# Kernel optimization log

Hardware: AMD Instinct MI355X
Metric: run time of the kernel (lower is better)

Reference implementation:

```python
import jax, jax.numpy as jnp
import numpy as np

B = 32768      # batch
D = 512        # embedding dim
V = 100000     # vocab_length (row 0 reserved -> table has V+1 rows)
S = 100        # num_neg_samples (hard-coded in source)
DISTORTION = 0.4


def _expected_counts():
    # fixed_unigram sampler: zipf-ish counts, distorted by 0.4, 1 reserved id
    counts = 1.0 / np.arange(1, V + 1, dtype=np.float64)
    p = counts ** DISTORTION
    p = p / p.sum()
    q = np.zeros(V + 1, dtype=np.float64)
    # unique sampling expected count: E[id in sample] = 1-(1-p)^S
    q[1:] = -np.expm1(S * np.log1p(-p))
    q[0] = 1e-9  # reserved id, never sampled; avoid log(0)
    return q


def setup_inputs() -> dict:
    key = jax.random.key(0)
    k1, k2, k3, k4 = jax.random.split(key, 4)
    label = jax.random.randint(k1, (B,), 1, V + 1, dtype=jnp.int64)
    inputs = jax.random.normal(k2, (B, D), dtype=jnp.float32)
    weights = jax.random.normal(k3, (V + 1, D), dtype=jnp.float32) * 0.05
    biases = jnp.zeros((V + 1,), dtype=jnp.float32)
    sampled_ids = jax.random.choice(k4, V, (S,), replace=False).astype(jnp.int64) + 1
    q = jnp.asarray(_expected_counts(), dtype=jnp.float32)
    true_expected_count = q[label]          # [B]
    sampled_expected_count = q[sampled_ids]  # [S]
    return {
        "label": label, "inputs": inputs, "weights": weights, "biases": biases,
        "sampled_ids": sampled_ids,
        "true_expected_count": true_expected_count,
        "sampled_expected_count": sampled_expected_count,
    }


def reference(label, inputs, weights, biases, sampled_ids,
              true_expected_count, sampled_expected_count):
    # --- _compute_sampled_logits with subtract_log_q=True ---
    true_w = weights[label]                                   # [B, D] gather
    true_logits = (jnp.einsum('bd,bd->b', inputs, true_w)
                   + biases[label]
                   - jnp.log(true_expected_count))            # [B]
    samp_w = weights[sampled_ids]                             # [S, D] gather
    samp_logits = (jnp.einsum('bd,sd->bs', inputs, samp_w)
                   + biases[sampled_ids]
                   - jnp.log(sampled_expected_count))         # [B, S]
    logits = jnp.concatenate([true_logits[:, None], samp_logits], axis=1)  # [B, 1+S]
    # labels are one-hot at column 0 -> CE = logsumexp - true logit
    losses = jax.nn.logsumexp(logits, axis=1) - logits[:, 0]
    loss = jnp.mean(losses)
    return logits, loss
```

## Files before the change

### kernel.cpp

```cpp
#include <hip/hip_runtime.h>
#include <math.h>

#define B_TOT 32768
#define DIM   512
#define NS    100
#define NCOL  101
#define TB    128
#define NBLK  (B_TOT / TB)
#define WPITCH 520

typedef __attribute__((ext_vector_type(8))) short short8;
typedef __attribute__((ext_vector_type(4))) float f32x4;

static __device__ __forceinline__ short f2bf(float f) {
    unsigned u = __builtin_bit_cast(unsigned, f);
    unsigned r = (u + 0x7FFFu + ((u >> 16) & 1u)) >> 16;
    return (short)r;
}

__global__ __launch_bounds__(512)
void fused_kernel(const int* __restrict__ label,
                  const float* __restrict__ inputs,
                  const float* __restrict__ weights,
                  const float* __restrict__ biases,
                  const int* __restrict__ sampled_ids,
                  const float* __restrict__ tq,
                  const float* __restrict__ sq,
                  float* __restrict__ out,
                  float* __restrict__ partial)
{
    __shared__ short W_lds[112 * WPITCH];
    __shared__ float base_lds[112];
    __shared__ float tl_lds[TB];
    __shared__ float ls_lds[8];

    const int t = threadIdx.x;

    for (int idx = t; idx < NS * (DIM / 4); idx += 512) {
        const int row = idx >> 7;
        const int kq  = (idx & 127) * 4;
        const float4 wv = *(const float4*)(weights + (long)sampled_ids[row] * DIM + kq);
        short4 p = make_short4(f2bf(wv.x), f2bf(wv.y), f2bf(wv.z), f2bf(wv.w));
        *(short4*)&W_lds[row * WPITCH + kq] = p;
    }
    if (t < 112)
        base_lds[t] = (t < NS) ? biases[sampled_ids[t]] - logf(sq[t]) : -INFINITY;

    const int wave = t >> 6;
    const int lane = t & 63;
    const int rit  = lane & 15;
    const int seg  = lane >> 4;
    const int absRow = blockIdx.x * TB + wave * 16 + rit;
    const int lab = label[absRow];
    const float* aptr = inputs  + (long)absRow * DIM + seg * 8;
    const float* wtp  = weights + (long)lab    * DIM + seg * 8;

    __syncthreads();

    f32x4 acc[7];
    #pragma unroll
    for (int c = 0; c < 7; c++) acc[c] = (f32x4){0.f, 0.f, 0.f, 0.f};
    float tacc = 0.f;

    #pragma unroll
    for (int kc = 0; kc < DIM / 32; kc++) {
        const int k0 = kc * 32;
        const float4 a0 = *(const float4*)(aptr + k0);
        const float4 a1 = *(const float4*)(aptr + k0 + 4);
        const float4 w0 = *(const float4*)(wtp + k0);
        const float4 w1 = *(const float4*)(wtp + k0 + 4);

        tacc = fmaf(a0.x, w0.x, tacc); tacc = fmaf(a0.y, w0.y, tacc);
        tacc = fmaf(a0.z, w0.z, tacc); tacc = fmaf(a0.w, w0.w, tacc);
        tacc = fmaf(a1.x, w1.x, tacc); tacc = fmaf(a1.y, w1.y, tacc);
        tacc = fmaf(a1.z, w1.z, tacc); tacc = fmaf(a1.w, w1.w, tacc);

        short8 af;
        af[0] = f2bf(a0.x); af[1] = f2bf(a0.y); af[2] = f2bf(a0.z); af[3] = f2bf(a0.w);
        af[4] = f2bf(a1.x); af[5] = f2bf(a1.y); af[6] = f2bf(a1.z); af[7] = f2bf(a1.w);

        const int wko = k0 + seg * 8;
        #pragma unroll
        for (int c = 0; c < 7; c++) {
            const short8 bf = *(const short8*)&W_lds[(c * 16 + rit) * WPITCH + wko];
            acc[c] = __builtin_amdgcn_mfma_f32_16x16x32_bf16(af, bf, acc[c], 0, 0, 0);
        }
    }

    tacc += __shfl_xor(tacc, 16);
    tacc += __shfl_xor(tacc, 32);
    const float tl = tacc + biases[lab] - logf(tq[absRow]);
    if (lane < 16) {
        tl_lds[wave * 16 + lane] = tl;
        out[(long)absRow * NCOL] = tl;
    }
    __syncthreads();

    const int g = lane >> 4;
    float loss_sum = 0.f;
    #pragma unroll
    for (int i = 0; i < 4; i++) {
        const int r = g * 4 + i;
        const long orow = (long)(blockIdx.x * TB + wave * 16 + r) * NCOL;
        const float tlv = tl_lds[wave * 16 + r];
        float v[7];
        float m = tlv;
        #pragma unroll
        for (int c = 0; c < 7; c++) {
            const int col = c * 16 + rit;
            v[c] = (col < NS) ? acc[c][i] + base_lds[col] : -INFINITY;
            m = fmaxf(m, v[c]);
        }
        #pragma unroll
        for (int off = 1; off < 16; off <<= 1) m = fmaxf(m, __shfl_xor(m, off));
        float s = (rit == 0) ? expf(tlv - m) : 0.f;
        #pragma unroll
        for (int c = 0; c < 7; c++) s += expf(v[c] - m);
        #pragma unroll
        for (int off = 1; off < 16; off <<= 1) s += __shfl_xor(s, off);
        loss_sum += m + logf(s) - tlv;
        #pragma unroll
        for (int c = 0; c < 7; c++) {
            const int col = c * 16 + rit;
            if (col < NS) out[orow + 1 + col] = v[c];
        }
    }
    float wl = (rit == 0) ? loss_sum : 0.f;
    wl += __shfl_xor(wl, 16);
    wl += __shfl_xor(wl, 32);
    if (lane == 0) ls_lds[wave] = wl;
    __syncthreads();
    if (t == 0) {
        float bp = 0.f;
        #pragma unroll
        for (int w = 0; w < 8; w++) bp += ls_lds[w];
        partial[blockIdx.x] = bp;
    }
}

__global__ __launch_bounds__(256)
void reduce_kernel(const float* __restrict__ partial, float* __restrict__ out_loss)
{
    __shared__ double buf[256];
    buf[threadIdx.x] = (double)partial[threadIdx.x];
    __syncthreads();
    for (int o = 128; o > 0; o >>= 1) {
        if (threadIdx.x < o) buf[threadIdx.x] += buf[threadIdx.x + o];
        __syncthreads();
    }
    if (threadIdx.x == 0) *out_loss = (float)(buf[0] * (1.0 / (double)B_TOT));
}

extern "C" void kernel_launch(void* const* d_in, const int* in_sizes, int n_in,
                              void* d_out, int out_size, void* d_ws, size_t ws_size,
                              hipStream_t stream)
{
    const int*   label   = (const int*)d_in[0];
    const float* inputs  = (const float*)d_in[1];
    const float* weights = (const float*)d_in[2];
    const float* biases  = (const float*)d_in[3];
    const int*   sids    = (const int*)d_in[4];
    const float* tq      = (const float*)d_in[5];
    const float* sq      = (const float*)d_in[6];
    float* out     = (float*)d_out;
    float* partial = (float*)d_ws;

    fused_kernel<<<NBLK, 512, 0, stream>>>(label, inputs, weights, biases,
                                           sids, tq, sq, out, partial);
    reduce_kernel<<<1, 256, 0, stream>>>(partial, out + (long)B_TOT * NCOL);
}
```

Measured before the change: 40.74 us.

## Prepack sampled weights into MFMA fragment layout in a separate kernel

A new pack kernel gathers the sampled weight rows once, converts them to bf16 and stores them in global memory already arranged in the per-lane MFMA B-fragment order. The bias-minus-log-q terms are precomputed there too. The fused kernel then reads these fragments straight from global memory (L2-resident) instead of having every block gather and convert 100 rows into LDS. This removes the LDS footprint and the block barriers, which should raise occupancy (launch bounds now ask for 4 blocks). In exchange it adds a third kernel launch and per-iteration global loads in the MFMA loop.

```diff
diff --git a/kernel.cpp b/kernel.cpp
--- a/kernel.cpp
+++ b/kernel.cpp
@@ -7,7 +7,10 @@
 #define NCOL  101
 #define TB    128
 #define NBLK  (B_TOT / TB)
-#define WPITCH 520
+
+#define BASE_OFF 28672
+#define LPART_OFF 28800
+#define NPACK (16 * 7 * 64)
 
 typedef __attribute__((ext_vector_type(8))) short short8;
 typedef __attribute__((ext_vector_type(4))) float f32x4;
@@ -18,34 +21,42 @@
     return (short)r;
 }
 
-__global__ __launch_bounds__(512)
+__global__ __launch_bounds__(256)
+void pack_kernel(const float* __restrict__ weights, const float* __restrict__ biases,
+                 const int* __restrict__ sids, const float* __restrict__ sq,
+                 short* __restrict__ wpack, float* __restrict__ base_g)
+{
+    const int tid = blockIdx.x * 256 + threadIdx.x;
+    if (tid < 112)
+        base_g[tid] = (tid < NS) ? biases[sids[tid]] - logf(sq[tid]) : -INFINITY;
+    if (tid >= NPACK) return;
+    const int kc = tid / 448, rem = tid % 448;
+    const int c = rem >> 6, l = rem & 63;
+    const int col = c * 16 + (l & 15);
+    const int k   = kc * 32 + (l >> 4) * 8;
+    short8 v = (short8){0, 0, 0, 0, 0, 0, 0, 0};
+    if (col < NS) {
+        const float* src = weights + (long)sids[col] * DIM + k;
+        const float4 f0 = *(const float4*)src;
+        const float4 f1 = *(const float4*)(src + 4);
+        v[0] = f2bf(f0.x); v[1] = f2bf(f0.y); v[2] = f2bf(f0.z); v[3] = f2bf(f0.w);
+        v[4] = f2bf(f1.x); v[5] = f2bf(f1.y); v[6] = f2bf(f1.z); v[7] = f2bf(f1.w);
+    }
+    *(short8*)&wpack[(long)tid * 8] = v;
+}
+
+__global__ __launch_bounds__(512, 4)
 void fused_kernel(const int* __restrict__ label,
                   const float* __restrict__ inputs,
                   const float* __restrict__ weights,
                   const float* __restrict__ biases,
-                  const int* __restrict__ sampled_ids,
                   const float* __restrict__ tq,
-                  const float* __restrict__ sq,
+                  const short* __restrict__ wpack,
+                  const float* __restrict__ base_g,
                   float* __restrict__ out,
-                  float* __restrict__ partial)
+                  float* __restrict__ lpart)
 {
-    __shared__ short W_lds[112 * WPITCH];
-    __shared__ float base_lds[112];
-    __shared__ float tl_lds[TB];
-    __shared__ float ls_lds[8];
-
-    const int t = threadIdx.x;
-
-    for (int idx = t; idx < NS * (DIM / 4); idx += 512) {
-        const int row = idx >> 7;
-        const int kq  = (idx & 127) * 4;
-        const float4 wv = *(const float4*)(weights + (long)sampled_ids[row] * DIM + kq);
-        short4 p = make_short4(f2bf(wv.x), f2bf(wv.y), f2bf(wv.z), f2bf(wv.w));
-        *(short4*)&W_lds[row * WPITCH + kq] = p;
-    }
-    if (t < 112)
-        base_lds[t] = (t < NS) ? biases[sampled_ids[t]] - logf(sq[t]) : -INFINITY;
-
+    const int t    = threadIdx.x;
     const int wave = t >> 6;
     const int lane = t & 63;
     const int rit  = lane & 15;
@@ -55,7 +66,9 @@
     const float* aptr = inputs  + (long)absRow * DIM + seg * 8;
     const float* wtp  = weights + (long)lab    * DIM + seg * 8;
 
-    __syncthreads();
+    float base_v[7];
+    #pragma unroll
+    for (int c = 0; c < 7; c++) base_v[c] = base_g[c * 16 + rit];
 
     f32x4 acc[7];
     #pragma unroll
@@ -79,10 +92,10 @@
         af[0] = f2bf(a0.x); af[1] = f2bf(a0.y); af[2] = f2bf(a0.z); af[3] = f2bf(a0.w);
         af[4] = f2bf(a1.x); af[5] = f2bf(a1.y); af[6] = f2bf(a1.z); af[7] = f2bf(a1.w);
 
-        const int wko = k0 + seg * 8;
+        const short* wp = wpack + ((long)kc * 7 * 64 + lane) * 8;
         #pragma unroll
         for (int c = 0; c < 7; c++) {
-            const short8 bf = *(const short8*)&W_lds[(c * 16 + rit) * WPITCH + wko];
+            const short8 bf = *(const short8*)(wp + c * 64 * 8);
             acc[c] = __builtin_amdgcn_mfma_f32_16x16x32_bf16(af, bf, acc[c], 0, 0, 0);
         }
     }
@@ -90,11 +103,7 @@
     tacc += __shfl_xor(tacc, 16);
     tacc += __shfl_xor(tacc, 32);
     const float tl = tacc + biases[lab] - logf(tq[absRow]);
-    if (lane < 16) {
-        tl_lds[wave * 16 + lane] = tl;
-        out[(long)absRow * NCOL] = tl;
-    }
-    __syncthreads();
+    if (lane < 16) out[(long)absRow * NCOL] = tl;
 
     const int g = lane >> 4;
     float loss_sum = 0.f;
@@ -102,13 +111,12 @@
     for (int i = 0; i < 4; i++) {
         const int r = g * 4 + i;
         const long orow = (long)(blockIdx.x * TB + wave * 16 + r) * NCOL;
-        const float tlv = tl_lds[wave * 16 + r];
+        const float tlv = __shfl(tl, r);
         float v[7];
         float m = tlv;
         #pragma unroll
         for (int c = 0; c < 7; c++) {
-            const int col = c * 16 + rit;
-            v[c] = (col < NS) ? acc[c][i] + base_lds[col] : -INFINITY;
+            v[c] = acc[c][i] + base_v[c];
             m = fmaxf(m, v[c]);
         }
         #pragma unroll
@@ -128,21 +136,16 @@
     float wl = (rit == 0) ? loss_sum : 0.f;
     wl += __shfl_xor(wl, 16);
     wl += __shfl_xor(wl, 32);
-    if (lane == 0) ls_lds[wave] = wl;
-    __syncthreads();
-    if (t == 0) {
-        float bp = 0.f;
-        #pragma unroll
-        for (int w = 0; w < 8; w++) bp += ls_lds[w];
-        partial[blockIdx.x] = bp;
-    }
+    if (lane == 0) lpart[blockIdx.x * 8 + wave] = wl;
 }
 
 __global__ __launch_bounds__(256)
-void reduce_kernel(const float* __restrict__ partial, float* __restrict__ out_loss)
+void reduce_kernel(const float* __restrict__ lpart, float* __restrict__ out_loss)
 {
+    double s = 0.0;
+    for (int i = threadIdx.x; i < NBLK * 8; i += 256) s += (double)lpart[i];
     __shared__ double buf[256];
-    buf[threadIdx.x] = (double)partial[threadIdx.x];
+    buf[threadIdx.x] = s;
     __syncthreads();
     for (int o = 128; o > 0; o >>= 1) {
         if (threadIdx.x < o) buf[threadIdx.x] += buf[threadIdx.x + o];
@@ -162,10 +165,14 @@
     const int*   sids    = (const int*)d_in[4];
     const float* tq      = (const float*)d_in[5];
     const float* sq      = (const float*)d_in[6];
-    float* out     = (float*)d_out;
-    float* partial = (float*)d_ws;
+    float* out  = (float*)d_out;
+    float* ws_f = (float*)d_ws;
+    short* wpack  = (short*)d_ws;
+    float* base_g = ws_f + BASE_OFF;
+    float* lpart  = ws_f + LPART_OFF;
 
-    fused_kernel<<<NBLK, 512, 0, stream>>>(label, inputs, weights, biases,
-                                           sids, tq, sq, out, partial);
-    reduce_kernel<<<1, 256, 0, stream>>>(partial, out + (long)B_TOT * NCOL);
+    pack_kernel<<<28, 256, 0, stream>>>(weights, biases, sids, sq, wpack, base_g);
+    fused_kernel<<<NBLK, 512, 0, stream>>>(label, inputs, weights, biases, tq,
+                                           wpack, base_g, out, lpart);
+    reduce_kernel<<<1, 256, 0, stream>>>(lpart, out + (long)B_TOT * NCOL);
 }
```

Result: slower. 44.02 us (+8.1%).

## Replace separate loss reduce kernel with last-block atomic fixed-point reduction

Applied to the files above, without the earlier changes.

Removes the second reduce kernel launch. Each block now adds its loss partial as a fixed-point 64-bit integer to a global atomic, and the last block to take a ticket writes the mean. Smaller edits cache the sampled ids in shared memory, broadcast true logits by shuffle instead of through LDS (dropping one barrier), and hoist the base values into registers. A memset is added each call to reset the counter, and the fixed-point scaling limits loss precision and range.

```diff
diff --git a/kernel.cpp b/kernel.cpp
--- a/kernel.cpp
+++ b/kernel.cpp
@@ -8,6 +8,7 @@
 #define TB    128
 #define NBLK  (B_TOT / TB)
 #define WPITCH 520
+#define LSCALE 1048576.0f
 
 typedef __attribute__((ext_vector_type(8))) short short8;
 typedef __attribute__((ext_vector_type(4))) float f32x4;
@@ -23,44 +24,49 @@
                   const float* __restrict__ inputs,
                   const float* __restrict__ weights,
                   const float* __restrict__ biases,
-                  const int* __restrict__ sampled_ids,
+                  const int* __restrict__ sids,
                   const float* __restrict__ tq,
                   const float* __restrict__ sq,
                   float* __restrict__ out,
-                  float* __restrict__ partial)
+                  unsigned long long* __restrict__ acc,
+                  unsigned* __restrict__ ticket)
 {
     __shared__ short W_lds[112 * WPITCH];
     __shared__ float base_lds[112];
-    __shared__ float tl_lds[TB];
+    __shared__ int   s_sid[NS];
     __shared__ float ls_lds[8];
 
     const int t = threadIdx.x;
 
-    for (int idx = t; idx < NS * (DIM / 4); idx += 512) {
+    if (t < NS) s_sid[t] = sids[t];
+    __syncthreads();
+
+    for (int idx = t; idx < NS * 128; idx += 512) {
         const int row = idx >> 7;
         const int kq  = (idx & 127) * 4;
-        const float4 wv = *(const float4*)(weights + (long)sampled_ids[row] * DIM + kq);
-        short4 p = make_short4(f2bf(wv.x), f2bf(wv.y), f2bf(wv.z), f2bf(wv.w));
-        *(short4*)&W_lds[row * WPITCH + kq] = p;
+        const float4 wv = *(const float4*)(weights + (long)s_sid[row] * DIM + kq);
+        *(short4*)&W_lds[row * WPITCH + kq] =
+            make_short4(f2bf(wv.x), f2bf(wv.y), f2bf(wv.z), f2bf(wv.w));
     }
     if (t < 112)
-        base_lds[t] = (t < NS) ? biases[sampled_ids[t]] - logf(sq[t]) : -INFINITY;
+        base_lds[t] = (t < NS) ? biases[s_sid[t]] - logf(sq[t]) : -INFINITY;
 
     const int wave = t >> 6;
     const int lane = t & 63;
     const int rit  = lane & 15;
     const int seg  = lane >> 4;
-    const int absRow = blockIdx.x * TB + wave * 16 + rit;
+    const long b0  = (long)blockIdx.x * TB;
+    const long absRow = b0 + wave * 16 + rit;
     const int lab = label[absRow];
-    const float* aptr = inputs  + (long)absRow * DIM + seg * 8;
-    const float* wtp  = weights + (long)lab    * DIM + seg * 8;
+    const float* aptr = inputs  + absRow * DIM + seg * 8;
+    const float* wtp  = weights + (long)lab * DIM + seg * 8;
+
+    f32x4 acc_r[7];
+    #pragma unroll
+    for (int c = 0; c < 7; c++) acc_r[c] = (f32x4){0.f, 0.f, 0.f, 0.f};
+    float tacc = 0.f;
 
     __syncthreads();
-
-    f32x4 acc[7];
-    #pragma unroll
-    for (int c = 0; c < 7; c++) acc[c] = (f32x4){0.f, 0.f, 0.f, 0.f};
-    float tacc = 0.f;
 
     #pragma unroll
     for (int kc = 0; kc < DIM / 32; kc++) {
@@ -83,32 +89,31 @@
         #pragma unroll
         for (int c = 0; c < 7; c++) {
             const short8 bf = *(const short8*)&W_lds[(c * 16 + rit) * WPITCH + wko];
-            acc[c] = __builtin_amdgcn_mfma_f32_16x16x32_bf16(af, bf, acc[c], 0, 0, 0);
+            acc_r[c] = __builtin_amdgcn_mfma_f32_16x16x32_bf16(af, bf, acc_r[c], 0, 0, 0);
         }
     }
 
     tacc += __shfl_xor(tacc, 16);
     tacc += __shfl_xor(tacc, 32);
     const float tl = tacc + biases[lab] - logf(tq[absRow]);
-    if (lane < 16) {
-        tl_lds[wave * 16 + lane] = tl;
-        out[(long)absRow * NCOL] = tl;
-    }
-    __syncthreads();
+    if (lane < 16) out[absRow * NCOL] = tl;
 
     const int g = lane >> 4;
+    float base_v[7];
+    #pragma unroll
+    for (int c = 0; c < 7; c++) base_v[c] = base_lds[c * 16 + rit];
+
     float loss_sum = 0.f;
     #pragma unroll
     for (int i = 0; i < 4; i++) {
         const int r = g * 4 + i;
-        const long orow = (long)(blockIdx.x * TB + wave * 16 + r) * NCOL;
-        const float tlv = tl_lds[wave * 16 + r];
+        const long orow = (b0 + wave * 16 + r) * NCOL;
+        const float tlv = __shfl(tl, r);
         float v[7];
         float m = tlv;
         #pragma unroll
         for (int c = 0; c < 7; c++) {
-            const int col = c * 16 + rit;
-            v[c] = (col < NS) ? acc[c][i] + base_lds[col] : -INFINITY;
+            v[c] = acc_r[c][i] + base_v[c];
             m = fmaxf(m, v[c]);
         }
         #pragma unroll
@@ -130,25 +135,21 @@
     wl += __shfl_xor(wl, 32);
     if (lane == 0) ls_lds[wave] = wl;
     __syncthreads();
+
     if (t == 0) {
         float bp = 0.f;
         #pragma unroll
         for (int w = 0; w < 8; w++) bp += ls_lds[w];
-        partial[blockIdx.x] = bp;
+        atomicAdd(acc, (unsigned long long)llrintf(bp * LSCALE));
+        __threadfence();
+        const unsigned old = atomicAdd(ticket, 1u);
+        if (old == NBLK - 1) {
+            __threadfence();
+            const unsigned long long total = atomicAdd(acc, 0ULL);
+            out[(long)B_TOT * NCOL] =
+                (float)((double)total * (1.0 / ((double)LSCALE * (double)B_TOT)));
+        }
     }
-}
-
-__global__ __launch_bounds__(256)
-void reduce_kernel(const float* __restrict__ partial, float* __restrict__ out_loss)
-{
-    __shared__ double buf[256];
-    buf[threadIdx.x] = (double)partial[threadIdx.x];
-    __syncthreads();
-    for (int o = 128; o > 0; o >>= 1) {
-        if (threadIdx.x < o) buf[threadIdx.x] += buf[threadIdx.x + o];
-        __syncthreads();
-    }
-    if (threadIdx.x == 0) *out_loss = (float)(buf[0] * (1.0 / (double)B_TOT));
 }
 
 extern "C" void kernel_launch(void* const* d_in, const int* in_sizes, int n_in,
@@ -162,10 +163,11 @@
     const int*   sids    = (const int*)d_in[4];
     const float* tq      = (const float*)d_in[5];
     const float* sq      = (const float*)d_in[6];
-    float* out     = (float*)d_out;
-    float* partial = (float*)d_ws;
+    float* out = (float*)d_out;
+    unsigned long long* acc = (unsigned long long*)d_ws;
+    unsigned* ticket = (unsigned*)((char*)d_ws + 8);
 
+    hipMemsetAsync(d_ws, 0, 16, stream);
     fused_kernel<<<NBLK, 512, 0, stream>>>(label, inputs, weights, biases,
-                                           sids, tq, sq, out, partial);
-    reduce_kernel<<<1, 256, 0, stream>>>(partial, out + (long)B_TOT * NCOL);
+                                           sids, tq, sq, out, acc, ticket);
 }
```

Result: slower. 49.71 us (+22.0%).
